# Kernel tuning notes

Measured on AMD Instinct MI355X. Metric: run time of the kernel, lower is better.

## Reference

```python
import jax, jax.numpy as jnp
import numpy as np

N, F, H, L = 1536, 32, 64, 3  # num_nodes, num_features, hidden, num_layers
NEG_SLOPE = 0.01
BN_EPS = 1e-5


def _lrelu(x):
    return jnp.where(x >= 0, x, NEG_SLOPE * x)


def _gin_layer(x, src, tgt, eps, w1, b1, w2, b2, g, be):
    # scatter-add aggregation: out[tgt] += x[src] (source_to_target flow)
    agg = jax.ops.segment_sum(x[src], tgt, num_segments=N)
    h = (1.0 + eps) * x + agg
    h = jax.nn.relu(h @ w1 + b1)
    h = jax.nn.relu(h @ w2 + b2)
    # BatchNorm1d, training-mode (batch statistics, biased variance)
    mean = jnp.mean(h, axis=0)
    var = jnp.mean((h - mean) ** 2, axis=0)
    return (h - mean) * jax.lax.rsqrt(var + BN_EPS) * g + be


def setup_inputs() -> dict:
    key = jax.random.key(0)
    ks = iter(jax.random.split(key, 40))

    def rn(shape, scale=0.05):
        return jax.random.normal(next(ks), shape, dtype=jnp.float32) * scale

    inp = {
        "x": rn((N, F), 1.0),
        "node_features": rn((N, F), 1.0),
        # conv1: F -> H
        "c1_eps": jnp.zeros((), jnp.float32),
        "c1_w1": rn((F, H)), "c1_b1": jnp.zeros((H,), jnp.float32),
        "c1_w2": rn((H, H)), "c1_b2": jnp.zeros((H,), jnp.float32),
        "c1_g": jnp.ones((H,), jnp.float32), "c1_be": jnp.zeros((H,), jnp.float32),
        # L-1 additional GIN convs: H -> H (stacked)
        "cv_eps": jnp.zeros((L - 1,), jnp.float32),
        "cv_w1": rn((L - 1, H, H)), "cv_b1": jnp.zeros((L - 1, H), jnp.float32),
        "cv_w2": rn((L - 1, H, H)), "cv_b2": jnp.zeros((L - 1, H), jnp.float32),
        "cv_g": jnp.ones((L - 1, H), jnp.float32), "cv_be": jnp.zeros((L - 1, H), jnp.float32),
        # projection head
        "lin1_w": rn((H, H)), "lin1_b": jnp.zeros((H,), jnp.float32),
        "lin2_w": rn((H, F)), "lin2_b": jnp.zeros((F,), jnp.float32),
        # edge predictor: 2F -> H -> H -> H -> 1
        "ep_w1": rn((2 * F, H)), "ep_b1": jnp.zeros((H,), jnp.float32),
        "ep_w2": rn((H, H)), "ep_b2": jnp.zeros((H,), jnp.float32),
        "ep_w3": rn((H, H)), "ep_b3": jnp.zeros((H,), jnp.float32),
        "ep_w4": rn((H, 1)), "ep_b4": jnp.zeros((1,), jnp.float32),
    }
    return inp


def reference(x, node_features, c1_eps, c1_w1, c1_b1, c1_w2, c1_b2, c1_g, c1_be,
              cv_eps, cv_w1, cv_b1, cv_w2, cv_b2, cv_g, cv_be,
              lin1_w, lin1_b, lin2_w, lin2_b,
              ep_w1, ep_b1, ep_w2, ep_b2, ep_w3, ep_b3, ep_w4, ep_b4):
    # complete-graph upper-triangular edge list (matches torch.combinations order)
    src, tgt = jnp.triu_indices(N, k=1)
    h = node_features  # forward ignores input x
    xinit = h
    h = _lrelu(_gin_layer(h, src, tgt, c1_eps, c1_w1, c1_b1, c1_w2, c1_b2, c1_g, c1_be))
    for i in range(L - 1):
        h = _lrelu(_gin_layer(h, src, tgt, cv_eps[i], cv_w1[i], cv_b1[i],
                              cv_w2[i], cv_b2[i], cv_g[i], cv_be[i]))
    h = _lrelu(h @ lin1_w + lin1_b)
    h = _lrelu(h @ lin2_w + lin2_b)
    h = h + xinit  # [N, F]

    # edge predictor: gather -> MLP -> sigmoid over E edges
    ef = jnp.concatenate([h[src], h[tgt]], axis=-1)  # [E, 2F]
    e = jax.nn.relu(ef @ ep_w1 + ep_b1)
    e = jax.nn.relu(e @ ep_w2 + ep_b2)
    e = jax.nn.relu(e @ ep_w3 + ep_b3)
    e = jax.nn.sigmoid(e @ ep_w4 + ep_b4)[:, 0]  # [E]

    probs = jnp.zeros((N, N), dtype=h.dtype)
    probs = probs.at[src, tgt].set(e).at[tgt, src].set(e)
    return probs
```

## Files before the change

kernel.cpp:

```cpp
#include <hip/hip_runtime.h>
#include <math.h>

#define NN 1536
#define FF 32
#define HH 64
#define EE (NN*(NN-1)/2)
#define EBLK 2493
#define BN_EPS 1e-5f
#define SLOPE 0.01f

typedef _Float16 v8h  __attribute__((ext_vector_type(8)));
typedef __fp16   v2hf __attribute__((ext_vector_type(2)));
typedef float    f32x4 __attribute__((ext_vector_type(4)));

union V8H { v8h v; v2hf h2[4]; float4 f4; };

__device__ __forceinline__ float lrelu_f(float v){ return v >= 0.f ? v : SLOPE*v; }
__device__ __forceinline__ f32x4 lrelu4(f32x4 v) {
  f32x4 r;
#pragma unroll
  for (int j = 0; j < 4; ++j) r[j] = v[j] >= 0.f ? v[j] : SLOPE*v[j];
  return r;
}

template<int DIN, bool FIRST>
__global__ __launch_bounds__(512) void k_gin(
    const float* __restrict__ zin,
    const float* __restrict__ gg, const float* __restrict__ be,
    const float* __restrict__ eps_p,
    const float* __restrict__ W1, const float* __restrict__ b1,
    const float* __restrict__ W2, const float* __restrict__ b2,
    float* __restrict__ zout,
    const float* __restrict__ pw2, const float* __restrict__ pw3,
    _Float16* __restrict__ pwf) {
  int bid = blockIdx.x, tid = threadIdx.x;
  if (FIRST && bid >= 96) {
    int i = (bid - 96)*512 + tid;
    if (i < 8192) {
      int mat = i >> 12, r = i & 4095;
      int k = r >> 6, cout = r & 63;
      int m = cout >> 4, cc = cout & 15;
      int q, g, b;
      if (mat == 0) { q = k >> 5; g = (k >> 3) & 3; b = k & 7; }
      else { int mF = k >> 4; g = (k >> 2) & 3; int rr = k & 3; q = mF >> 1; b = ((mF & 1) << 2) | rr; }
      const float* W = mat ? pw3 : pw2;
      pwf[mat*4096 + ((q*4 + m)*64 + (g*16 + cc))*8 + b] = (_Float16)W[r];
    }
    return;
  }

  __shared__ float W1s[DIN*64];
  __shared__ float W2s[4096];
  __shared__ float red[2048];
  __shared__ float redq[2048];
  __shared__ float scl[64], sft[64], pf[64];
  __shared__ float hh[16][64];
  __shared__ float uls[16*64];
  __shared__ float t1s[16][64];

  int c = tid & 63, y = tid >> 6;
  for (int i = tid; i < DIN*64; i += 512) W1s[i] = W1[i];
  for (int i = tid; i < 4096; i += 512)   W2s[i] = W2[i];

  constexpr int C4 = DIN/4;
  constexpr int RS = 512/C4;
  int col4 = tid % C4, rseg = tid / C4;
  const f32x4* z4 = (const f32x4*)zin;
  int r0 = bid*16;

  if (!FIRST) {
    f32x4 s0 = {0.f,0.f,0.f,0.f}, s1 = s0, s2 = s0, s3 = s0;
    f32x4 q0 = s0, q1 = s0, q2 = s0, q3 = s0;
    for (int n = rseg; n < NN; n += 4*RS) {
      f32x4 v0 = z4[n*C4 + col4];
      f32x4 v1 = z4[(n + RS)*C4 + col4];
      f32x4 v2 = z4[(n + 2*RS)*C4 + col4];
      f32x4 v3 = z4[(n + 3*RS)*C4 + col4];
      s0 += v0; q0 += v0*v0;
      s1 += v1; q1 += v1*v1;
      s2 += v2; q2 += v2*v2;
      s3 += v3; q3 += v3*v3;
    }
    f32x4 s4 = (s0 + s1) + (s2 + s3);
    f32x4 q4 = (q0 + q1) + (q2 + q3);
#pragma unroll
    for (int j = 0; j < 4; ++j) {
      red[rseg*DIN + col4*4 + j]  = s4[j];
      redq[rseg*DIN + col4*4 + j] = q4[j];
    }
    __syncthreads();
    if (tid < DIN) {
      float S = 0.f, Q = 0.f;
      for (int r = 0; r < RS; ++r) { S += red[r*DIN + tid]; Q += redq[r*DIN + tid]; }
      float m  = S * (1.f/NN);
      float iv = rsqrtf(Q * (1.f/NN) - m*m + BN_EPS);
      float sc = iv * gg[tid];
      scl[tid] = sc;
      sft[tid] = be[tid] - m*sc;
    }
    __syncthreads();
  }

  {
    f32x4 p0 = {0.f,0.f,0.f,0.f}, p1 = p0;
    f32x4 sc4, sh4;
    if (!FIRST) {
#pragma unroll
      for (int j = 0; j < 4; ++j) { sc4[j] = scl[col4*4 + j]; sh4[j] = sft[col4*4 + j]; }
    }
    int n = rseg;
    for (; n + RS < r0; n += 2*RS) {
      f32x4 va = z4[n*C4 + col4];
      f32x4 vb = z4[(n + RS)*C4 + col4];
      if (!FIRST) { va = lrelu4(va*sc4 + sh4); vb = lrelu4(vb*sc4 + sh4); }
      p0 += va; p1 += vb;
    }
    for (; n < r0; n += RS) {
      f32x4 va = z4[n*C4 + col4];
      if (!FIRST) va = lrelu4(va*sc4 + sh4);
      p0 += va;
    }
    p0 += p1;
#pragma unroll
    for (int j = 0; j < 4; ++j) red[rseg*DIN + col4*4 + j] = p0[j];
    __syncthreads();
    if (tid < DIN) {
      float S = 0.f;
      for (int r = 0; r < RS; ++r) S += red[r*DIN + tid];
      pf[tid] = S;
    }
    __syncthreads();
  }

  float e1 = 1.f + eps_p[0];
  if (c < DIN) {
    for (int rr = y; rr < 16; rr += 8) {
      float v = zin[(r0 + rr)*DIN + c];
      hh[rr][c] = FIRST ? v : lrelu_f(v*scl[c] + sft[c]);
    }
  }
  __syncthreads();
  if (c < DIN) {
    for (int rr = y; rr < 16; rr += 8) {
      float run = pf[c];
      for (int r2 = 0; r2 < rr; ++r2) run += hh[r2][c];
      uls[rr*DIN + c] = e1*hh[rr][c] + run;
    }
  }
  __syncthreads();

  {
    float a0 = b1[c], a1 = a0;
    for (int k = 0; k < DIN; ++k) {
      float w = W1s[k*64 + c];
      a0 = fmaf(uls[y*DIN + k],       w, a0);
      a1 = fmaf(uls[(y + 8)*DIN + k], w, a1);
    }
    t1s[y][c]     = fmaxf(a0, 0.f);
    t1s[y + 8][c] = fmaxf(a1, 0.f);
  }
  __syncthreads();

  {
    float z0 = b2[c], z1 = z0;
    for (int k = 0; k < 64; ++k) {
      float w = W2s[k*64 + c];
      z0 = fmaf(t1s[y][k],     w, z0);
      z1 = fmaf(t1s[y + 8][k], w, z1);
    }
    zout[(r0 + y)*64 + c]     = fmaxf(z0, 0.f);
    zout[(r0 + y + 8)*64 + c] = fmaxf(z1, 0.f);
  }
}

__global__ __launch_bounds__(512) void k_head(
    const float* __restrict__ z,
    const float* __restrict__ gg, const float* __restrict__ be,
    const float* __restrict__ l1w, const float* __restrict__ l1b,
    const float* __restrict__ l2w, const float* __restrict__ l2b,
    const float* __restrict__ nf,
    const float* __restrict__ epw1, const float* __restrict__ epb1,
    _Float16* __restrict__ Ah, _Float16* __restrict__ Bh) {
  __shared__ float W1s[4096];
  __shared__ float W2s[2048];
  __shared__ float Was[2048];
  __shared__ float Wbs[2048];
  __shared__ float scratch[4096];
  __shared__ float scl[64], sft[64];
  int tid = threadIdx.x, c = tid & 63, y = tid >> 6;
  for (int i = tid; i < 4096; i += 512) W1s[i] = l1w[i];
  for (int i = tid; i < 2048; i += 512) { W2s[i] = l2w[i]; Was[i] = epw1[i]; Wbs[i] = epw1[2048 + i]; }

  {
    int col4 = tid & 15, rseg = tid >> 4;
    const f32x4* z4 = (const f32x4*)z;
    f32x4 s0 = {0.f,0.f,0.f,0.f}, s1 = s0, s2 = s0, s3 = s0;
    f32x4 q0 = s0, q1 = s0, q2 = s0, q3 = s0;
    for (int n = rseg; n < NN; n += 128) {
      f32x4 v0 = z4[n*16 + col4];
      f32x4 v1 = z4[(n + 32)*16 + col4];
      f32x4 v2 = z4[(n + 64)*16 + col4];
      f32x4 v3 = z4[(n + 96)*16 + col4];
      s0 += v0; q0 += v0*v0;
      s1 += v1; q1 += v1*v1;
      s2 += v2; q2 += v2*v2;
      s3 += v3; q3 += v3*v3;
    }
    f32x4 s4 = (s0 + s1) + (s2 + s3);
    f32x4 q4 = (q0 + q1) + (q2 + q3);
    float* red  = scratch;
    float* redq = scratch + 2048;
#pragma unroll
    for (int j = 0; j < 4; ++j) {
      red[rseg*64 + col4*4 + j]  = s4[j];
      redq[rseg*64 + col4*4 + j] = q4[j];
    }
    __syncthreads();
    if (tid < 64) {
      float S = 0.f, Q = 0.f;
      for (int r = 0; r < 32; ++r) { S += red[r*64 + tid]; Q += redq[r*64 + tid]; }
      float m  = S * (1.f/NN);
      float iv = rsqrtf(Q * (1.f/NN) - m*m + BN_EPS);
      float sc = iv * gg[tid];
      scl[tid] = sc;
      sft[tid] = be[tid] - m*sc;
    }
    __syncthreads();
  }

  float* t0 = scratch;
  float* t1 = scratch + 1024;
  float* t2 = scratch + 2048;
  int r0 = blockIdx.x*16;

  for (int rr = y; rr < 16; rr += 8)
    t0[rr*64 + c] = lrelu_f(z[(r0 + rr)*64 + c]*scl[c] + sft[c]);
  __syncthreads();
  {
    float a0 = l1b[c], a1 = a0;
    for (int k = 0; k < 64; ++k) {
      float w = W1s[k*64 + c];
      a0 = fmaf(t0[y*64 + k],       w, a0);
      a1 = fmaf(t0[(y + 8)*64 + k], w, a1);
    }
    t1[y*64 + c]       = lrelu_f(a0);
    t1[(y + 8)*64 + c] = lrelu_f(a1);
  }
  __syncthreads();
  if (c < 32) {
    float v0 = l2b[c], v1 = v0;
    for (int k = 0; k < 64; ++k) {
      float w = W2s[k*32 + c];
      v0 = fmaf(t1[y*64 + k],       w, v0);
      v1 = fmaf(t1[(y + 8)*64 + k], w, v1);
    }
    t2[y*32 + c]       = lrelu_f(v0) + nf[(r0 + y)*32 + c];
    t2[(y + 8)*32 + c] = lrelu_f(v1) + nf[(r0 + y + 8)*32 + c];
  }
  __syncthreads();
  {
    float av0 = epb1[c], av1 = av0;
    float bv0 = 0.f, bv1 = 0.f;
    for (int k = 0; k < 32; ++k) {
      float wa = Was[k*64 + c], wb = Wbs[k*64 + c];
      av0 = fmaf(t2[y*32 + k], wa, av0);       bv0 = fmaf(t2[y*32 + k], wb, bv0);
      av1 = fmaf(t2[(y + 8)*32 + k], wa, av1); bv1 = fmaf(t2[(y + 8)*32 + k], wb, bv1);
    }
    Ah[(r0 + y)*64 + c]     = (_Float16)av0;  Bh[(r0 + y)*64 + c]     = (_Float16)bv0;
    Ah[(r0 + y + 8)*64 + c] = (_Float16)av1;  Bh[(r0 + y + 8)*64 + c] = (_Float16)bv1;
  }
}

__global__ __launch_bounds__(256, 3) void k_edges_f16(
    const _Float16* __restrict__ Ah, const _Float16* __restrict__ Bh,
    const _Float16* __restrict__ Wf,
    const float* __restrict__ b2, const float* __restrict__ b3,
    const float* __restrict__ w4, const float* __restrict__ b4,
    float* __restrict__ out) {
  int tid = threadIdx.x, wid = tid >> 6, lane = tid & 63;
  int c = lane & 15, g = lane >> 4;

  int w = blockIdx.x*4 + wid;
  int cum, kk, sbase;
  if (w < 1524) { cum = 0; kk = 12; sbase = 0; }
  else {
    cum = 1524; kk = 11; sbase = 127;
    while (kk > 1 && w >= cum + 128*kk) { cum += 128*kk; sbase += 128; --kk; }
  }
  int idx = w - cum;
  int q = idx / kk;
  int s = sbase + q;
  int t0 = s + 1 + ((idx - q*kk) << 7);

  const v8h* wp = (const v8h*)Wf;
  v8h wv2[8], wv3[8];
#pragma unroll
  for (int f = 0; f < 8; ++f) { wv2[f] = wp[f*64 + lane]; wv3[f] = wp[512 + f*64 + lane]; }

  f32x4 b2v[4], b3v[4];
  v2hf w4h[8];
  int g4 = g*4;
#pragma unroll
  for (int m = 0; m < 4; ++m) {
#pragma unroll
    for (int r = 0; r < 4; ++r) {
      int f = 16*m + g4 + r;
      b2v[m][r] = b2[f]; b3v[m][r] = b3[f];
    }
    v2hf wa = { (__fp16)w4[16*m + g4],     (__fp16)w4[16*m + g4 + 1] };
    v2hf wb = { (__fp16)w4[16*m + g4 + 2], (__fp16)w4[16*m + g4 + 3] };
    w4h[2*m] = wa; w4h[2*m + 1] = wb;
  }
  float b4v = b4[0];

  V8H zu; zu.f4 = make_float4(0.f, 0.f, 0.f, 0.f);
  const v8h vzero = zu.v;
  const v2hf z2 = { (__fp16)0.f, (__fp16)0.f };

  V8H a0, a1;
  a0.f4 = *(const float4*)(Ah + s*64 + g*8);
  a1.f4 = *(const float4*)(Ah + s*64 + 32 + g*8);

  int tl = t0 + c;
  V8H y0, y1;
  y0.f4 = *(const float4*)(Bh + tl*64 + g*8);
  y1.f4 = *(const float4*)(Bh + tl*64 + 32 + g*8);

  for (int it = 0; it < 8; ++it) {
    int tb = t0 + (it << 4);
    if (tb >= NN) break;
    int t = tb + c;

    V8H f0, f1;
    f0.v = __builtin_elementwise_max(a0.v + y0.v, vzero);
    f1.v = __builtin_elementwise_max(a1.v + y1.v, vzero);

    int tn = tb + 16 + c;
    y0.f4 = *(const float4*)(Bh + tn*64 + g*8);
    y1.f4 = *(const float4*)(Bh + tn*64 + 32 + g*8);

    __builtin_amdgcn_s_setprio(1);
    f32x4 acc[4];
#pragma unroll
    for (int m = 0; m < 4; ++m)
      acc[m] = __builtin_amdgcn_mfma_f32_16x16x32_f16(wv2[m],     f0.v, b2v[m], 0, 0, 0);
#pragma unroll
    for (int m = 0; m < 4; ++m)
      acc[m] = __builtin_amdgcn_mfma_f32_16x16x32_f16(wv2[4 + m], f1.v, acc[m], 0, 0, 0);
    __builtin_amdgcn_s_setprio(0);

    V8H p0, p1;
#pragma unroll
    for (int m = 0; m < 2; ++m) {
      p0.h2[2*m]     = __builtin_elementwise_max(__builtin_amdgcn_cvt_pkrtz(acc[m][0],   acc[m][1]),   z2);
      p0.h2[2*m + 1] = __builtin_elementwise_max(__builtin_amdgcn_cvt_pkrtz(acc[m][2],   acc[m][3]),   z2);
      p1.h2[2*m]     = __builtin_elementwise_max(__builtin_amdgcn_cvt_pkrtz(acc[m+2][0], acc[m+2][1]), z2);
      p1.h2[2*m + 1] = __builtin_elementwise_max(__builtin_amdgcn_cvt_pkrtz(acc[m+2][2], acc[m+2][3]), z2);
    }

    __builtin_amdgcn_s_setprio(1);
    f32x4 acc3[4];
#pragma unroll
    for (int m = 0; m < 4; ++m)
      acc3[m] = __builtin_amdgcn_mfma_f32_16x16x32_f16(wv3[m],     p0.v, b3v[m], 0, 0, 0);
#pragma unroll
    for (int m = 0; m < 4; ++m)
      acc3[m] = __builtin_amdgcn_mfma_f32_16x16x32_f16(wv3[4 + m], p1.v, acc3[m], 0, 0, 0);
    __builtin_amdgcn_s_setprio(0);

    float p = 0.f;
#pragma unroll
    for (int m = 0; m < 4; ++m) {
      v2hf l0 = __builtin_elementwise_max(
          __builtin_amdgcn_cvt_pkrtz(acc3[m][0], acc3[m][1]), z2);
      v2hf l1 = __builtin_elementwise_max(
          __builtin_amdgcn_cvt_pkrtz(acc3[m][2], acc3[m][3]), z2);
      p = __builtin_amdgcn_fdot2(l0, w4h[2*m],     p, false);
      p = __builtin_amdgcn_fdot2(l1, w4h[2*m + 1], p, false);
    }
    p += __shfl_xor(p, 16, 64);
    p += __shfl_xor(p, 32, 64);
    float ez = __builtin_amdgcn_exp2f(-1.44269504f * (p + b4v));
    float prob = __builtin_amdgcn_rcpf(1.f + ez);
    if (lane < 16 && t < NN) out[s*NN + t] = prob;
  }
}

__global__ __launch_bounds__(256) void k_mirror(float* __restrict__ out) {
  __shared__ float tile[32][33];
  int k = blockIdx.x;
  int bi = (int)((sqrtf(8.f*k + 1.f) - 1.f)*0.5f);
  while (bi*(bi + 1)/2 > k) --bi;
  while ((bi + 1)*(bi + 2)/2 <= k) ++bi;
  int bj = k - bi*(bi + 1)/2;
  int i0 = bi*32, j0 = bj*32;
  int tx = threadIdx.x & 31, ty = threadIdx.x >> 5;
#pragma unroll
  for (int r = 0; r < 4; ++r)
    tile[ty + r*8][tx] = out[(j0 + ty + r*8)*NN + i0 + tx];
  __syncthreads();
#pragma unroll
  for (int r = 0; r < 4; ++r) {
    int row = ty + r*8;
    int i = i0 + row, j = j0 + tx;
    if (bi > bj)      out[i*NN + j] = tile[tx][row];
    else if (i > j)   out[i*NN + j] = tile[tx][row];
    else if (i == j)  out[i*NN + j] = 0.f;
  }
}

extern "C" void kernel_launch(void* const* d_in, const int* in_sizes, int n_in,
                              void* d_out, int out_size, void* d_ws, size_t ws_size,
                              hipStream_t stream) {
  const float* nf     = (const float*)d_in[1];
  const float* c1_eps = (const float*)d_in[2];
  const float* c1_w1  = (const float*)d_in[3];
  const float* c1_b1  = (const float*)d_in[4];
  const float* c1_w2  = (const float*)d_in[5];
  const float* c1_b2  = (const float*)d_in[6];
  const float* c1_g   = (const float*)d_in[7];
  const float* c1_be  = (const float*)d_in[8];
  const float* cv_eps = (const float*)d_in[9];
  const float* cv_w1  = (const float*)d_in[10];
  const float* cv_b1  = (const float*)d_in[11];
  const float* cv_w2  = (const float*)d_in[12];
  const float* cv_b2  = (const float*)d_in[13];
  const float* cv_g   = (const float*)d_in[14];
  const float* cv_be  = (const float*)d_in[15];
  const float* lin1_w = (const float*)d_in[16];
  const float* lin1_b = (const float*)d_in[17];
  const float* lin2_w = (const float*)d_in[18];
  const float* lin2_b = (const float*)d_in[19];
  const float* ep_w1  = (const float*)d_in[20];
  const float* ep_b1  = (const float*)d_in[21];
  const float* ep_w2  = (const float*)d_in[22];
  const float* ep_b2  = (const float*)d_in[23];
  const float* ep_w3  = (const float*)d_in[24];
  const float* ep_b3  = (const float*)d_in[25];
  const float* ep_w4  = (const float*)d_in[26];
  const float* ep_b4  = (const float*)d_in[27];

  float* ws = (float*)d_ws;
  float* zA    = ws;
  float* zB    = zA + NN*64;
  _Float16* Ah = (_Float16*)(zB + NN*64);
  _Float16* Bh = Ah + NN*64;
  _Float16* Wf = Bh + NN*64;

  float* out = (float*)d_out;

  k_gin<32, true><<<112, 512, 0, stream>>>(nf, nullptr, nullptr, c1_eps,
      c1_w1, c1_b1, c1_w2, c1_b2, zA, ep_w2, ep_w3, Wf);

  k_gin<64, false><<<96, 512, 0, stream>>>(zA, c1_g, c1_be, cv_eps,
      cv_w1, cv_b1, cv_w2, cv_b2, zB, nullptr, nullptr, nullptr);

  k_gin<64, false><<<96, 512, 0, stream>>>(zB, cv_g, cv_be, cv_eps + 1,
      cv_w1 + HH*HH, cv_b1 + HH, cv_w2 + HH*HH, cv_b2 + HH, zA,
      nullptr, nullptr, nullptr);

  k_head<<<96, 512, 0, stream>>>(zA, cv_g + HH, cv_be + HH,
                                 lin1_w, lin1_b, lin2_w, lin2_b, nf,
                                 ep_w1, ep_b1, Ah, Bh);

  k_edges_f16<<<EBLK, 256, 0, stream>>>(Ah, Bh, Wf, ep_b2, ep_b3, ep_w4, ep_b4, out);

  k_mirror<<<1176, 256, 0, stream>>>(out);
}
```

Measured before the change: 89.00 us.

## Stage edge-MLP weights in LDS to raise occupancy; unroll column-sum loop

The edge kernel no longer holds the 64x64 layer-2 and layer-3 fp16 weight fragments in registers. It copies them into a 16KB shared-memory buffer and reads them per MFMA inside the loop, and launch bounds go from 3 to 4 blocks per CU. The aim is to cut VGPR pressure so more waves are resident to hide memory latency, at the cost of extra LDS reads on every iteration and a block barrier. Separately, the GIN column-sum loop is unrolled from 2 to 4 accumulators to expose more memory-level parallelism.

```diff
diff --git a/kernel.cpp b/kernel.cpp
--- a/kernel.cpp
+++ b/kernel.cpp
@@ -102,25 +102,30 @@
   }
 
   {
-    f32x4 p0 = {0.f,0.f,0.f,0.f}, p1 = p0;
+    f32x4 p0 = {0.f,0.f,0.f,0.f}, p1 = p0, p2 = p0, p3 = p0;
     f32x4 sc4, sh4;
     if (!FIRST) {
 #pragma unroll
       for (int j = 0; j < 4; ++j) { sc4[j] = scl[col4*4 + j]; sh4[j] = sft[col4*4 + j]; }
     }
     int n = rseg;
-    for (; n + RS < r0; n += 2*RS) {
+    for (; n + 3*RS < r0; n += 4*RS) {
       f32x4 va = z4[n*C4 + col4];
       f32x4 vb = z4[(n + RS)*C4 + col4];
-      if (!FIRST) { va = lrelu4(va*sc4 + sh4); vb = lrelu4(vb*sc4 + sh4); }
-      p0 += va; p1 += vb;
+      f32x4 vc = z4[(n + 2*RS)*C4 + col4];
+      f32x4 vd = z4[(n + 3*RS)*C4 + col4];
+      if (!FIRST) {
+        va = lrelu4(va*sc4 + sh4); vb = lrelu4(vb*sc4 + sh4);
+        vc = lrelu4(vc*sc4 + sh4); vd = lrelu4(vd*sc4 + sh4);
+      }
+      p0 += va; p1 += vb; p2 += vc; p3 += vd;
     }
     for (; n < r0; n += RS) {
       f32x4 va = z4[n*C4 + col4];
       if (!FIRST) va = lrelu4(va*sc4 + sh4);
       p0 += va;
     }
-    p0 += p1;
+    p0 = (p0 + p1) + (p2 + p3);
 #pragma unroll
     for (int j = 0; j < 4; ++j) red[rseg*DIN + col4*4 + j] = p0[j];
     __syncthreads();
@@ -271,14 +276,21 @@
   }
 }
 
-__global__ __launch_bounds__(256, 3) void k_edges_f16(
+__global__ __launch_bounds__(256, 4) void k_edges_f16(
     const _Float16* __restrict__ Ah, const _Float16* __restrict__ Bh,
     const _Float16* __restrict__ Wf,
     const float* __restrict__ b2, const float* __restrict__ b3,
     const float* __restrict__ w4, const float* __restrict__ b4,
     float* __restrict__ out) {
+  __shared__ _Float16 Wl[8192];
   int tid = threadIdx.x, wid = tid >> 6, lane = tid & 63;
   int c = lane & 15, g = lane >> 4;
+
+  {
+    const float4* src = (const float4*)Wf;
+    float4* dst = (float4*)Wl;
+    for (int i = tid; i < 1024; i += 256) dst[i] = src[i];
+  }
 
   int w = blockIdx.x*4 + wid;
   int cum, kk, sbase;
@@ -292,11 +304,6 @@
   int s = sbase + q;
   int t0 = s + 1 + ((idx - q*kk) << 7);
 
-  const v8h* wp = (const v8h*)Wf;
-  v8h wv2[8], wv3[8];
-#pragma unroll
-  for (int f = 0; f < 8; ++f) { wv2[f] = wp[f*64 + lane]; wv3[f] = wp[512 + f*64 + lane]; }
-
   f32x4 b2v[4], b3v[4];
   v2hf w4h[8];
   int g4 = g*4;
@@ -326,6 +333,9 @@
   y0.f4 = *(const float4*)(Bh + tl*64 + g*8);
   y1.f4 = *(const float4*)(Bh + tl*64 + 32 + g*8);
 
+  const v8h* wl = (const v8h*)Wl;
+  __syncthreads();
+
   for (int it = 0; it < 8; ++it) {
     int tb = t0 + (it << 4);
     if (tb >= NN) break;
@@ -343,10 +353,10 @@
     f32x4 acc[4];
 #pragma unroll
     for (int m = 0; m < 4; ++m)
-      acc[m] = __builtin_amdgcn_mfma_f32_16x16x32_f16(wv2[m],     f0.v, b2v[m], 0, 0, 0);
+      acc[m] = __builtin_amdgcn_mfma_f32_16x16x32_f16(wl[m*64 + lane], f0.v, b2v[m], 0, 0, 0);
 #pragma unroll
     for (int m = 0; m < 4; ++m)
-      acc[m] = __builtin_amdgcn_mfma_f32_16x16x32_f16(wv2[4 + m], f1.v, acc[m], 0, 0, 0);
+      acc[m] = __builtin_amdgcn_mfma_f32_16x16x32_f16(wl[(4 + m)*64 + lane], f1.v, acc[m], 0, 0, 0);
     __builtin_amdgcn_s_setprio(0);
 
     V8H p0, p1;
@@ -362,10 +372,10 @@
     f32x4 acc3[4];
 #pragma unroll
     for (int m = 0; m < 4; ++m)
-      acc3[m] = __builtin_amdgcn_mfma_f32_16x16x32_f16(wv3[m],     p0.v, b3v[m], 0, 0, 0);
+      acc3[m] = __builtin_amdgcn_mfma_f32_16x16x32_f16(wl[512 + m*64 + lane], p0.v, b3v[m], 0, 0, 0);
 #pragma unroll
     for (int m = 0; m < 4; ++m)
-      acc3[m] = __builtin_amdgcn_mfma_f32_16x16x32_f16(wv3[4 + m], p1.v, acc3[m], 0, 0, 0);
+      acc3[m] = __builtin_amdgcn_mfma_f32_16x16x32_f16(wl[512 + (4 + m)*64 + lane], p1.v, acc3[m], 0, 0, 0);
     __builtin_amdgcn_s_setprio(0);
 
     float p = 0.f;
```

Result: faster. 87.04 us (-2.2%).
